# Performance work log

Hardware: AMD Instinct MI355X
Metric: run time of the kernel (lower is better)

Reference implementation:

```python
import jax, jax.numpy as jnp
import numpy as np

GAMMA = 1.0  # RBF kernel width (init kwarg gamma)
N_PAIRS = 8_388_608
N_LAYERS = 8


def setup_inputs() -> dict:
    key = jax.random.key(0)
    ks = jax.random.split(key, 12)
    inp = {
        "x": jax.random.normal(ks[0], (N_PAIRS, 2), dtype=jnp.float32),
        "y": jax.random.normal(ks[1], (N_PAIRS, 2), dtype=jnp.float32),
        # input layer (clip=False)
        "W0": jax.random.normal(ks[2], (2, 2), dtype=jnp.float32),
        "b0": jax.random.normal(ks[3], (2,), dtype=jnp.float32),
        "scale0": jax.random.uniform(ks[4], (2,), dtype=jnp.float32),
        "shift0": jax.random.normal(ks[5], (2,), dtype=jnp.float32),
        # hidden layers (weights/biases clipped to [-5, 5] at construction)
        "Ws": jnp.clip(jax.random.normal(ks[6], (N_LAYERS, 2, 2), dtype=jnp.float32), -5.0, 5.0),
        "bs": jnp.clip(jax.random.normal(ks[7], (N_LAYERS, 2), dtype=jnp.float32), -5.0, 5.0),
        "scales": jax.random.uniform(ks[8], (N_LAYERS, 2), dtype=jnp.float32),
        "shifts": jax.random.normal(ks[9], (N_LAYERS, 2), dtype=jnp.float32),
        # final head Linear(2, 1)
        "Wf": jax.random.normal(ks[10], (1, 2), dtype=jnp.float32),
        "bf": jax.random.normal(ks[11], (1,), dtype=jnp.float32),
    }
    return inp


def _fraud_net(z, W0, b0, scale0, shift0, Ws, bs, scales, shifts, Wf, bf):
    # input layer: tanh(Linear(2,2)) * scale + shift   (z: [N,2])
    z = jnp.tanh(z @ W0.T + b0) * scale0 + shift0

    def step(z, p):
        W, b, s, t = p
        return jnp.tanh(z @ W.T + b) * s + t, None

    z, _ = jax.lax.scan(step, z, (Ws, bs, scales, shifts))
    # final Linear(2, 1) then squeeze -> [N]
    return (z @ Wf.T + bf)[..., 0]


def reference(x, y, W0, b0, scale0, shift0, Ws, bs, scales, shifts, Wf, bf):
    diff = x - y  # [N, 2]
    rbf = jnp.exp(-GAMMA * jnp.sum(diff * diff, axis=-1))  # [N]
    fx = _fraud_net(x, W0, b0, scale0, shift0, Ws, bs, scales, shifts, Wf, bf)
    fy = _fraud_net(y, W0, b0, scale0, shift0, Ws, bs, scales, shifts, Wf, bf)
    return rbf * fx * fy  # [N]
```

## Files before the change

kernel.cpp:

```cpp
#include <hip/hip_runtime.h>
#include <math.h>

#define N_LAYERS 8
#define TAB 48
#define TABSZ (TAB * TAB)
#define LOG2E2 2.8853900817779268f
#define NLOG2E 1.4426950408889634f
#define UCLAMP 24.0f
#define BLK 512

#if __has_builtin(__builtin_amdgcn_exp2f)
__device__ __forceinline__ float exp2_fast(float x) { return __builtin_amdgcn_exp2f(x); }
#else
__device__ __forceinline__ float exp2_fast(float x) { return __expf(0.6931471805599453f * x); }
#endif


__global__ __launch_bounds__(1024) void setup_all(
    const float* __restrict__ W0, const float* __restrict__ b0,
    const float* __restrict__ s0, const float* __restrict__ t0,
    const float* __restrict__ Ws, const float* __restrict__ bs,
    const float* __restrict__ ss, const float* __restrict__ ts,
    const float* __restrict__ Wf, const float* __restrict__ bf,
    float* __restrict__ fp, float4* __restrict__ gt4) {
    __shared__ float gs[TABSZ];
    __shared__ float fs[16];

    if (threadIdx.x == 0) {
        fs[0] = LOG2E2 * W0[0]; fs[1] = LOG2E2 * W0[1];
        fs[2] = LOG2E2 * W0[2]; fs[3] = LOG2E2 * W0[3];
        fs[4] = LOG2E2 * b0[0]; fs[5] = LOG2E2 * b0[1];
        for (int c = 0; c < 2; ++c) {
            float s = s0[c], t = t0[c];
            float span = fmaxf(2.2f * s, 1e-5f);
            float h  = span / (float)(TAB - 1);
            float lo = t - 0.5f * span;
            float ih = (float)(TAB - 1) / span;
            fs[6 + c]  = (s + 0.5f * span) * ih;
            fs[8 + c]  = 2.0f * s * ih;
            fs[10 + c] = lo;
            fs[12 + c] = h;
        }
        for (int i = 0; i < 14; ++i) fp[i] = fs[i];
    }
    __syncthreads();

    for (int idx = threadIdx.x; idx < TABSZ; idx += blockDim.x) {
        int k1 = idx / TAB, k0 = idx - k1 * TAB;
        float z0 = fs[10] + (float)k0 * fs[12];
        float z1 = fs[11] + (float)k1 * fs[13];
        for (int l = 0; l < N_LAYERS; ++l) {
            float u0 = fmaf(z0, Ws[4 * l + 0], fmaf(z1, Ws[4 * l + 1], bs[2 * l + 0]));
            float u1 = fmaf(z0, Ws[4 * l + 2], fmaf(z1, Ws[4 * l + 3], bs[2 * l + 1]));
            z0 = fmaf(tanhf(u0), ss[2 * l + 0], ts[2 * l + 0]);
            z1 = fmaf(tanhf(u1), ss[2 * l + 1], ts[2 * l + 1]);
        }
        gs[idx] = fmaf(z0, Wf[0], fmaf(z1, Wf[1], bf[0]));
    }
    __syncthreads();

    for (int idx = threadIdx.x; idx < TABSZ; idx += blockDim.x) {
        int iy = idx / TAB, ix = idx - iy * TAB;
        const float* row = gs + iy * TAB;
        int c0 = max(ix - 1, 0);
        int c1 = ix;
        int c2 = min(ix + 1, TAB - 1);
        int c3 = min(ix + 2, TAB - 1);
        gt4[idx] = make_float4(row[c0], row[c1], row[c2], row[c3]);
    }
}

__device__ __forceinline__ void cr_w(float f, float w[4]) {
    w[0] = f * fmaf(f, fmaf(f, -0.5f, 1.0f), -0.5f);
    w[1] = fmaf(f * f, fmaf(f, 1.5f, -2.5f), 1.0f);
    w[2] = f * fmaf(f, fmaf(f, -1.5f, 2.0f), 0.5f);
    w[3] = f * f * fmaf(f, 0.5f, -0.5f);
}

__device__ __forceinline__ float interp_two(const float4* __restrict__ tab4,
                                            float ax0, float ax1, float ay0, float ay1) {
    int ixa = min(max((int)ax0, 1), TAB - 3);
    int iya = min(max((int)ax1, 1), TAB - 3);
    int ixb = min(max((int)ay0, 1), TAB - 3);
    int iyb = min(max((int)ay1, 1), TAB - 3);
    float fxa = ax0 - (float)ixa, fya = ax1 - (float)iya;
    float fxb = ay0 - (float)ixb, fyb = ay1 - (float)iyb;

    const float4* pa = tab4 + (iya - 1) * TAB + ixa;
    const float4* pb = tab4 + (iyb - 1) * TAB + ixb;
    float4 a0 = pa[0], a1 = pa[TAB], a2 = pa[2 * TAB], a3 = pa[3 * TAB];
    float4 b0 = pb[0], b1 = pb[TAB], b2 = pb[2 * TAB], b3 = pb[3 * TAB];

    float wxa[4], wya[4], wxb[4], wyb[4];
    cr_w(fxa, wxa); cr_w(fya, wya);
    cr_w(fxb, wxb); cr_w(fyb, wyb);

    float ra0 = fmaf(a0.w, wxa[3], fmaf(a0.z, wxa[2], fmaf(a0.y, wxa[1], a0.x * wxa[0])));
    float ra1 = fmaf(a1.w, wxa[3], fmaf(a1.z, wxa[2], fmaf(a1.y, wxa[1], a1.x * wxa[0])));
    float ra2 = fmaf(a2.w, wxa[3], fmaf(a2.z, wxa[2], fmaf(a2.y, wxa[1], a2.x * wxa[0])));
    float ra3 = fmaf(a3.w, wxa[3], fmaf(a3.z, wxa[2], fmaf(a3.y, wxa[1], a3.x * wxa[0])));
    float gx  = fmaf(ra3, wya[3], fmaf(ra2, wya[2], fmaf(ra1, wya[1], ra0 * wya[0])));

    float rb0 = fmaf(b0.w, wxb[3], fmaf(b0.z, wxb[2], fmaf(b0.y, wxb[1], b0.x * wxb[0])));
    float rb1 = fmaf(b1.w, wxb[3], fmaf(b1.z, wxb[2], fmaf(b1.y, wxb[1], b1.x * wxb[0])));
    float rb2 = fmaf(b2.w, wxb[3], fmaf(b2.z, wxb[2], fmaf(b2.y, wxb[1], b2.x * wxb[0])));
    float rb3 = fmaf(b3.w, wxb[3], fmaf(b3.z, wxb[2], fmaf(b3.y, wxb[1], b3.x * wxb[0])));
    float gy  = fmaf(rb3, wyb[3], fmaf(rb2, wyb[2], fmaf(rb1, wyb[1], rb0 * wyb[0])));

    return gx * gy;
}

__device__ __forceinline__ float pair_val(const float4* __restrict__ tab4,
                                          float px0, float px1, float py0, float py1,
                                          float C0, float C1, float D0, float D1) {
    float d0 = exp2_fast(fminf(px0, UCLAMP)) + 1.0f;
    float d1 = exp2_fast(fminf(px1, UCLAMP)) + 1.0f;
    float d2 = exp2_fast(fminf(py0, UCLAMP)) + 1.0f;
    float d3 = exp2_fast(fminf(py1, UCLAMP)) + 1.0f;
    float p2 = d0 * d1, p3 = p2 * d2, p4 = p3 * d3;
    float R = __builtin_amdgcn_rcpf(p4);
    float i3 = R * p3;  R *= d3;
    float i2 = R * p2;  R *= d2;
    float i1 = R * d0;
    float i0 = R * d1;
    float ux0 = fmaf(-D0, i0, C0), ux1 = fmaf(-D1, i1, C1);
    float uy0 = fmaf(-D0, i2, C0), uy1 = fmaf(-D1, i3, C1);
    return interp_two(tab4, ux0, ux1, uy0, uy1);
}

__global__ __launch_bounds__(BLK, 8) void fraud_kernel(
    const float4* __restrict__ x4, const float4* __restrict__ y4,
    const float* __restrict__ fp, const float4* __restrict__ gt4,
    float2* __restrict__ out2, int stride)
{
    __shared__ float4 tab4[TABSZ];
    for (int j = threadIdx.x; j < TABSZ; j += BLK) tab4[j] = gt4[j];
    __syncthreads();

    float Wt0 = fp[0], Wt1 = fp[1], Wt2 = fp[2], Wt3 = fp[3];
    float bt0 = fp[4], bt1 = fp[5];
    float C0 = fp[6], C1 = fp[7], D0 = fp[8], D1 = fp[9];

    int tid = blockIdx.x * BLK + threadIdx.x;
#pragma unroll
    for (int k = 0; k < 4; ++k) {
        int g = tid + k * stride;
        float4 xa = x4[g], ya = y4[g];

        float pxa0 = fmaf(xa.x, Wt0, fmaf(xa.y, Wt1, bt0));
        float pxa1 = fmaf(xa.x, Wt2, fmaf(xa.y, Wt3, bt1));
        float pya0 = fmaf(ya.x, Wt0, fmaf(ya.y, Wt1, bt0));
        float pya1 = fmaf(ya.x, Wt2, fmaf(ya.y, Wt3, bt1));
        float dxA = xa.x - ya.x, dyA = xa.y - ya.y;
        float rA = exp2_fast(-NLOG2E * fmaf(dxA, dxA, dyA * dyA));
        float resA = rA * pair_val(tab4, pxa0, pxa1, pya0, pya1, C0, C1, D0, D1);

        float pxb0 = fmaf(xa.z, Wt0, fmaf(xa.w, Wt1, bt0));
        float pxb1 = fmaf(xa.z, Wt2, fmaf(xa.w, Wt3, bt1));
        float pyb0 = fmaf(ya.z, Wt0, fmaf(ya.w, Wt1, bt0));
        float pyb1 = fmaf(ya.z, Wt2, fmaf(ya.w, Wt3, bt1));
        float dxB = xa.z - ya.z, dyB = xa.w - ya.w;
        float rB = exp2_fast(-NLOG2E * fmaf(dxB, dxB, dyB * dyB));
        float resB = rB * pair_val(tab4, pxb0, pxb1, pyb0, pyb1, C0, C1, D0, D1);

        out2[g] = make_float2(resA, resB);
    }
}

extern "C" void kernel_launch(void* const* d_in, const int* in_sizes, int n_in,
                              void* d_out, int out_size, void* d_ws, size_t ws_size,
                              hipStream_t stream) {
    const float* x  = (const float*)d_in[0];
    const float* y  = (const float*)d_in[1];
    const float* W0 = (const float*)d_in[2];
    const float* b0 = (const float*)d_in[3];
    const float* s0 = (const float*)d_in[4];
    const float* t0 = (const float*)d_in[5];
    const float* Ws = (const float*)d_in[6];
    const float* bs = (const float*)d_in[7];
    const float* ss = (const float*)d_in[8];
    const float* ts = (const float*)d_in[9];
    const float* Wf = (const float*)d_in[10];
    const float* bf = (const float*)d_in[11];
    float* out = (float*)d_out;
    float* fp  = (float*)d_ws;
    float4* gt4 = (float4*)(fp + 16);

    hipLaunchKernelGGL(setup_all, dim3(1), dim3(1024), 0, stream,
                       W0, b0, s0, t0, Ws, bs, ss, ts, Wf, bf, fp, gt4);

    int n       = out_size;
    int ngroups = n / 2;
    int threads = ngroups / 4;
    dim3 block(BLK);
    dim3 grid(threads / BLK);
    hipLaunchKernelGGL(fraud_kernel, grid, block, 0, stream,
                       (const float4*)x, (const float4*)y, fp, gt4,
                       (float2*)out, threads);
}
```

Baseline: 186.2 us.

## Software-pipeline LDS table reads and prefetch inputs with sched barriers; parallelize table setup

The main kernel is manually interleaved: the table gathers for one half-pair are issued while arithmetic for the other half proceeds, and sched_barrier calls pin that order so the compiler cannot regroup it. The next iteration's x/y loads are prefetched into registers ahead of use, hiding global memory latency. The setup kernel now runs one block per table row (48 blocks) instead of a single 1024-thread block, shortening the serial setup phase. The risks are higher register pressure and losing the compiler's own scheduling choices.

```diff
diff --git a/kernel.cpp b/kernel.cpp
--- a/kernel.cpp
+++ b/kernel.cpp
@@ -15,18 +15,26 @@
 __device__ __forceinline__ float exp2_fast(float x) { return __expf(0.6931471805599453f * x); }
 #endif
 
-
-__global__ __launch_bounds__(1024) void setup_all(
+#if __has_builtin(__builtin_amdgcn_sched_barrier)
+#define SB() __builtin_amdgcn_sched_barrier(0)
+#else
+#define SB()
+#endif
+
+
+__global__ __launch_bounds__(64) void setup48(
     const float* __restrict__ W0, const float* __restrict__ b0,
     const float* __restrict__ s0, const float* __restrict__ t0,
     const float* __restrict__ Ws, const float* __restrict__ bs,
     const float* __restrict__ ss, const float* __restrict__ ts,
     const float* __restrict__ Wf, const float* __restrict__ bf,
     float* __restrict__ fp, float4* __restrict__ gt4) {
-    __shared__ float gs[TABSZ];
     __shared__ float fs[16];
-
-    if (threadIdx.x == 0) {
+    __shared__ float row[TAB];
+    int iy = blockIdx.x;
+    int tx = threadIdx.x;
+
+    if (tx == 0) {
         fs[0] = LOG2E2 * W0[0]; fs[1] = LOG2E2 * W0[1];
         fs[2] = LOG2E2 * W0[2]; fs[3] = LOG2E2 * W0[3];
         fs[4] = LOG2E2 * b0[0]; fs[5] = LOG2E2 * b0[1];
@@ -41,32 +49,29 @@
             fs[10 + c] = lo;
             fs[12 + c] = h;
         }
-        for (int i = 0; i < 14; ++i) fp[i] = fs[i];
+        if (iy == 0)
+            for (int i = 0; i < 14; ++i) fp[i] = fs[i];
     }
     __syncthreads();
 
-    for (int idx = threadIdx.x; idx < TABSZ; idx += blockDim.x) {
-        int k1 = idx / TAB, k0 = idx - k1 * TAB;
-        float z0 = fs[10] + (float)k0 * fs[12];
-        float z1 = fs[11] + (float)k1 * fs[13];
+    if (tx < TAB) {
+        float z0 = fs[10] + (float)tx * fs[12];
+        float z1 = fs[11] + (float)iy * fs[13];
         for (int l = 0; l < N_LAYERS; ++l) {
             float u0 = fmaf(z0, Ws[4 * l + 0], fmaf(z1, Ws[4 * l + 1], bs[2 * l + 0]));
             float u1 = fmaf(z0, Ws[4 * l + 2], fmaf(z1, Ws[4 * l + 3], bs[2 * l + 1]));
             z0 = fmaf(tanhf(u0), ss[2 * l + 0], ts[2 * l + 0]);
             z1 = fmaf(tanhf(u1), ss[2 * l + 1], ts[2 * l + 1]);
         }
-        gs[idx] = fmaf(z0, Wf[0], fmaf(z1, Wf[1], bf[0]));
+        row[tx] = fmaf(z0, Wf[0], fmaf(z1, Wf[1], bf[0]));
     }
     __syncthreads();
 
-    for (int idx = threadIdx.x; idx < TABSZ; idx += blockDim.x) {
-        int iy = idx / TAB, ix = idx - iy * TAB;
-        const float* row = gs + iy * TAB;
-        int c0 = max(ix - 1, 0);
-        int c1 = ix;
-        int c2 = min(ix + 1, TAB - 1);
-        int c3 = min(ix + 2, TAB - 1);
-        gt4[idx] = make_float4(row[c0], row[c1], row[c2], row[c3]);
+    if (tx < TAB) {
+        int c0 = max(tx - 1, 0);
+        int c2 = min(tx + 1, TAB - 1);
+        int c3 = min(tx + 2, TAB - 1);
+        gt4[iy * TAB + tx] = make_float4(row[c0], row[tx], row[c2], row[c3]);
     }
 }
 
@@ -77,55 +82,8 @@
     w[3] = f * f * fmaf(f, 0.5f, -0.5f);
 }
 
-__device__ __forceinline__ float interp_two(const float4* __restrict__ tab4,
-                                            float ax0, float ax1, float ay0, float ay1) {
-    int ixa = min(max((int)ax0, 1), TAB - 3);
-    int iya = min(max((int)ax1, 1), TAB - 3);
-    int ixb = min(max((int)ay0, 1), TAB - 3);
-    int iyb = min(max((int)ay1, 1), TAB - 3);
-    float fxa = ax0 - (float)ixa, fya = ax1 - (float)iya;
-    float fxb = ay0 - (float)ixb, fyb = ay1 - (float)iyb;
-
-    const float4* pa = tab4 + (iya - 1) * TAB + ixa;
-    const float4* pb = tab4 + (iyb - 1) * TAB + ixb;
-    float4 a0 = pa[0], a1 = pa[TAB], a2 = pa[2 * TAB], a3 = pa[3 * TAB];
-    float4 b0 = pb[0], b1 = pb[TAB], b2 = pb[2 * TAB], b3 = pb[3 * TAB];
-
-    float wxa[4], wya[4], wxb[4], wyb[4];
-    cr_w(fxa, wxa); cr_w(fya, wya);
-    cr_w(fxb, wxb); cr_w(fyb, wyb);
-
-    float ra0 = fmaf(a0.w, wxa[3], fmaf(a0.z, wxa[2], fmaf(a0.y, wxa[1], a0.x * wxa[0])));
-    float ra1 = fmaf(a1.w, wxa[3], fmaf(a1.z, wxa[2], fmaf(a1.y, wxa[1], a1.x * wxa[0])));
-    float ra2 = fmaf(a2.w, wxa[3], fmaf(a2.z, wxa[2], fmaf(a2.y, wxa[1], a2.x * wxa[0])));
-    float ra3 = fmaf(a3.w, wxa[3], fmaf(a3.z, wxa[2], fmaf(a3.y, wxa[1], a3.x * wxa[0])));
-    float gx  = fmaf(ra3, wya[3], fmaf(ra2, wya[2], fmaf(ra1, wya[1], ra0 * wya[0])));
-
-    float rb0 = fmaf(b0.w, wxb[3], fmaf(b0.z, wxb[2], fmaf(b0.y, wxb[1], b0.x * wxb[0])));
-    float rb1 = fmaf(b1.w, wxb[3], fmaf(b1.z, wxb[2], fmaf(b1.y, wxb[1], b1.x * wxb[0])));
-    float rb2 = fmaf(b2.w, wxb[3], fmaf(b2.z, wxb[2], fmaf(b2.y, wxb[1], b2.x * wxb[0])));
-    float rb3 = fmaf(b3.w, wxb[3], fmaf(b3.z, wxb[2], fmaf(b3.y, wxb[1], b3.x * wxb[0])));
-    float gy  = fmaf(rb3, wyb[3], fmaf(rb2, wyb[2], fmaf(rb1, wyb[1], rb0 * wyb[0])));
-
-    return gx * gy;
-}
-
-__device__ __forceinline__ float pair_val(const float4* __restrict__ tab4,
-                                          float px0, float px1, float py0, float py1,
-                                          float C0, float C1, float D0, float D1) {
-    float d0 = exp2_fast(fminf(px0, UCLAMP)) + 1.0f;
-    float d1 = exp2_fast(fminf(px1, UCLAMP)) + 1.0f;
-    float d2 = exp2_fast(fminf(py0, UCLAMP)) + 1.0f;
-    float d3 = exp2_fast(fminf(py1, UCLAMP)) + 1.0f;
-    float p2 = d0 * d1, p3 = p2 * d2, p4 = p3 * d3;
-    float R = __builtin_amdgcn_rcpf(p4);
-    float i3 = R * p3;  R *= d3;
-    float i2 = R * p2;  R *= d2;
-    float i1 = R * d0;
-    float i0 = R * d1;
-    float ux0 = fmaf(-D0, i0, C0), ux1 = fmaf(-D1, i1, C1);
-    float uy0 = fmaf(-D0, i2, C0), uy1 = fmaf(-D1, i3, C1);
-    return interp_two(tab4, ux0, ux1, uy0, uy1);
+__device__ __forceinline__ float dot4(float4 t, const float w[4]) {
+    return fmaf(t.w, w[3], fmaf(t.z, w[2], fmaf(t.y, w[1], t.x * w[0])));
 }
 
 __global__ __launch_bounds__(BLK, 8) void fraud_kernel(
@@ -142,28 +100,102 @@
     float C0 = fp[6], C1 = fp[7], D0 = fp[8], D1 = fp[9];
 
     int tid = blockIdx.x * BLK + threadIdx.x;
+    float4 xa = x4[tid], ya = y4[tid];
 #pragma unroll
     for (int k = 0; k < 4; ++k) {
         int g = tid + k * stride;
-        float4 xa = x4[g], ya = y4[g];
 
         float pxa0 = fmaf(xa.x, Wt0, fmaf(xa.y, Wt1, bt0));
         float pxa1 = fmaf(xa.x, Wt2, fmaf(xa.y, Wt3, bt1));
         float pya0 = fmaf(ya.x, Wt0, fmaf(ya.y, Wt1, bt0));
         float pya1 = fmaf(ya.x, Wt2, fmaf(ya.y, Wt3, bt1));
-        float dxA = xa.x - ya.x, dyA = xa.y - ya.y;
-        float rA = exp2_fast(-NLOG2E * fmaf(dxA, dxA, dyA * dyA));
-        float resA = rA * pair_val(tab4, pxa0, pxa1, pya0, pya1, C0, C1, D0, D1);
-
+        float dA0 = exp2_fast(fminf(pxa0, UCLAMP)) + 1.0f;
+        float dA1 = exp2_fast(fminf(pxa1, UCLAMP)) + 1.0f;
+        float dA2 = exp2_fast(fminf(pya0, UCLAMP)) + 1.0f;
+        float dA3 = exp2_fast(fminf(pya1, UCLAMP)) + 1.0f;
+        float p2A = dA0 * dA1, p3A = p2A * dA2, p4A = p3A * dA3;
+        float RA = __builtin_amdgcn_rcpf(p4A);
+        float iA3 = RA * p3A;  RA *= dA3;
+        float iA2 = RA * p2A;  RA *= dA2;
+        float iA1 = RA * dA0;
+        float iA0 = RA * dA1;
+        float uxA0 = fmaf(-D0, iA0, C0), uxA1 = fmaf(-D1, iA1, C1);
+        float uyA0 = fmaf(-D0, iA2, C0), uyA1 = fmaf(-D1, iA3, C1);
+        int ixAx = min(max((int)uxA0, 1), TAB - 3);
+        int iyAx = min(max((int)uxA1, 1), TAB - 3);
+        int ixAy = min(max((int)uyA0, 1), TAB - 3);
+        int iyAy = min(max((int)uyA1, 1), TAB - 3);
+        float fxAx = uxA0 - (float)ixAx, fyAx = uxA1 - (float)iyAx;
+        float fxAy = uyA0 - (float)ixAy, fyAy = uyA1 - (float)iyAy;
+        const float4* pAx = tab4 + (iyAx - 1) * TAB + ixAx;
+        const float4* pAy = tab4 + (iyAy - 1) * TAB + ixAy;
+        SB();
+        float4 ax0 = pAx[0], ax1 = pAx[TAB], ax2 = pAx[2 * TAB], ax3 = pAx[3 * TAB];
+        SB();
         float pxb0 = fmaf(xa.z, Wt0, fmaf(xa.w, Wt1, bt0));
         float pxb1 = fmaf(xa.z, Wt2, fmaf(xa.w, Wt3, bt1));
         float pyb0 = fmaf(ya.z, Wt0, fmaf(ya.w, Wt1, bt0));
         float pyb1 = fmaf(ya.z, Wt2, fmaf(ya.w, Wt3, bt1));
+        float dB0 = exp2_fast(fminf(pxb0, UCLAMP)) + 1.0f;
+        float dB1 = exp2_fast(fminf(pxb1, UCLAMP)) + 1.0f;
+        float dB2 = exp2_fast(fminf(pyb0, UCLAMP)) + 1.0f;
+        float dB3 = exp2_fast(fminf(pyb1, UCLAMP)) + 1.0f;
+        float p2B = dB0 * dB1, p3B = p2B * dB2, p4B = p3B * dB3;
+        float RB = __builtin_amdgcn_rcpf(p4B);
+        float iB3 = RB * p3B;  RB *= dB3;
+        float iB2 = RB * p2B;  RB *= dB2;
+        float iB1 = RB * dB0;
+        float iB0 = RB * dB1;
+        float uxB0 = fmaf(-D0, iB0, C0), uxB1 = fmaf(-D1, iB1, C1);
+        float uyB0 = fmaf(-D0, iB2, C0), uyB1 = fmaf(-D1, iB3, C1);
+        int ixBx = min(max((int)uxB0, 1), TAB - 3);
+        int iyBx = min(max((int)uxB1, 1), TAB - 3);
+        int ixBy = min(max((int)uyB0, 1), TAB - 3);
+        int iyBy = min(max((int)uyB1, 1), TAB - 3);
+        float fxBx = uxB0 - (float)ixBx, fyBx = uxB1 - (float)iyBx;
+        float fxBy = uyB0 - (float)ixBy, fyBy = uyB1 - (float)iyBy;
+        const float4* pBx = tab4 + (iyBx - 1) * TAB + ixBx;
+        const float4* pBy = tab4 + (iyBy - 1) * TAB + ixBy;
+        float dxA = xa.x - ya.x, dyA = xa.y - ya.y;
+        float rA = exp2_fast(-NLOG2E * fmaf(dxA, dxA, dyA * dyA));
         float dxB = xa.z - ya.z, dyB = xa.w - ya.w;
         float rB = exp2_fast(-NLOG2E * fmaf(dxB, dxB, dyB * dyB));
-        float resB = rB * pair_val(tab4, pxb0, pxb1, pyb0, pyb1, C0, C1, D0, D1);
-
+        SB();
+        float4 ay0 = pAy[0], ay1 = pAy[TAB], ay2 = pAy[2 * TAB], ay3 = pAy[3 * TAB];
+        SB();
+        float wxAx[4], wyAx[4], wxAy[4], wyAy[4];
+        cr_w(fxAx, wxAx); cr_w(fyAx, wyAx);
+        cr_w(fxAy, wxAy); cr_w(fyAy, wyAy);
+        SB();
+        float ra0 = dot4(ax0, wxAx), ra1 = dot4(ax1, wxAx);
+        float ra2 = dot4(ax2, wxAx), ra3 = dot4(ax3, wxAx);
+        float gxA = fmaf(ra3, wyAx[3], fmaf(ra2, wyAx[2], fmaf(ra1, wyAx[1], ra0 * wyAx[0])));
+        SB();
+        float4 bx0 = pBx[0], bx1 = pBx[TAB], bx2 = pBx[2 * TAB], bx3 = pBx[3 * TAB];
+        SB();
+        float sa0 = dot4(ay0, wxAy), sa1 = dot4(ay1, wxAy);
+        float sa2 = dot4(ay2, wxAy), sa3 = dot4(ay3, wxAy);
+        float gyA = fmaf(sa3, wyAy[3], fmaf(sa2, wyAy[2], fmaf(sa1, wyAy[1], sa0 * wyAy[0])));
+        float resA = rA * (gxA * gyA);
+        SB();
+        float wxBx[4], wyBx[4], wxBy[4], wyBy[4];
+        cr_w(fxBx, wxBx); cr_w(fyBx, wyBx);
+        cr_w(fxBy, wxBy); cr_w(fyBy, wyBy);
+        float4 xn, yn;
+        if (k < 3) { int gn = g + stride; xn = x4[gn]; yn = y4[gn]; }
+        SB();
+        float4 by0 = pBy[0], by1 = pBy[TAB], by2 = pBy[2 * TAB], by3 = pBy[3 * TAB];
+        SB();
+        float rb0 = dot4(bx0, wxBx), rb1 = dot4(bx1, wxBx);
+        float rb2 = dot4(bx2, wxBx), rb3 = dot4(bx3, wxBx);
+        float gxB = fmaf(rb3, wyBx[3], fmaf(rb2, wyBx[2], fmaf(rb1, wyBx[1], rb0 * wyBx[0])));
+        SB();
+        float sb0 = dot4(by0, wxBy), sb1 = dot4(by1, wxBy);
+        float sb2 = dot4(by2, wxBy), sb3 = dot4(by3, wxBy);
+        float gyB = fmaf(sb3, wyBy[3], fmaf(sb2, wyBy[2], fmaf(sb1, wyBy[1], sb0 * wyBy[0])));
+        float resB = rB * (gxB * gyB);
         out2[g] = make_float2(resA, resB);
+        if (k < 3) { xa = xn; ya = yn; }
     }
 }
 
@@ -186,7 +218,7 @@
     float* fp  = (float*)d_ws;
     float4* gt4 = (float4*)(fp + 16);
 
-    hipLaunchKernelGGL(setup_all, dim3(1), dim3(1024), 0, stream,
+    hipLaunchKernelGGL(setup48, dim3(TAB), dim3(64), 0, stream,
                        W0, b0, s0, t0, Ws, bs, ss, ts, Wf, bf, fp, gt4);
 
     int n       = out_size;
```

Result: slower. 477.5 us (+156.5%).
